# Kernel optimization log

Measured on AMD Instinct MI355X. Metric: run time of the kernel, lower is better.

The kernel has to match this reference:

```python
import jax, jax.numpy as jnp
import numpy as np

N_NODES = 100000
N_EDGES = 3200000
F_IN = 128
HID = 32
N_CLASSES = 40
NEG_SLOPE = 0.2


def _add_self_loops(edge_index, n):
    loops = jnp.arange(n, dtype=edge_index.dtype)
    src = jnp.concatenate([edge_index[0], loops])
    dst = jnp.concatenate([edge_index[1], loops])
    return src, dst


def _gat_layer(x, src, dst, W, a_src, a_dst, b, n):
    # h: [N, C]
    h = x @ W
    hs = h[src]                      # [E, C] gathered source features
    alpha_s = hs @ a_src             # [E]
    alpha_d = (h @ a_dst)[dst]       # [E]
    e = jax.nn.leaky_relu(alpha_s + alpha_d, NEG_SLOPE)
    # segment softmax over incoming edges per destination node
    m = jax.ops.segment_max(e, dst, num_segments=n)
    ex = jnp.exp(e - m[dst])
    denom = jax.ops.segment_sum(ex, dst, num_segments=n)
    alpha = ex / denom[dst]
    out = jax.ops.segment_sum(alpha[:, None] * hs, dst, num_segments=n)
    return out + b


def setup_inputs() -> dict:
    key = jax.random.key(0)
    ks = jax.random.split(key, 8)
    x = jax.random.normal(ks[0], (N_NODES, F_IN), dtype=jnp.float32)
    edge_index = jax.random.randint(ks[1], (2, N_EDGES), 0, N_NODES, dtype=jnp.int32)
    W1 = jax.random.normal(ks[2], (F_IN, HID), dtype=jnp.float32) * (1.0 / np.sqrt(F_IN))
    att_src1 = jax.random.normal(ks[3], (HID,), dtype=jnp.float32) * 0.1
    att_dst1 = jax.random.normal(ks[4], (HID,), dtype=jnp.float32) * 0.1
    b1 = jnp.zeros((HID,), dtype=jnp.float32)
    W2 = jax.random.normal(ks[5], (HID, N_CLASSES), dtype=jnp.float32) * (1.0 / np.sqrt(HID))
    att_src2 = jax.random.normal(ks[6], (N_CLASSES,), dtype=jnp.float32) * 0.1
    att_dst2 = jax.random.normal(ks[7], (N_CLASSES,), dtype=jnp.float32) * 0.1
    b2 = jnp.zeros((N_CLASSES,), dtype=jnp.float32)
    return {"x": x, "edge_index": edge_index, "W1": W1, "att_src1": att_src1,
            "att_dst1": att_dst1, "b1": b1, "W2": W2, "att_src2": att_src2,
            "att_dst2": att_dst2, "b2": b2}


def reference(x, edge_index, W1, att_src1, att_dst1, b1, W2, att_src2, att_dst2, b2):
    n = x.shape[0]
    src, dst = _add_self_loops(edge_index, n)  # PyG GATConv default add_self_loops=True
    h = _gat_layer(x, src, dst, W1, att_src1, att_dst1, b1, n)
    h = jax.nn.relu(h)  # dropout is identity in eval mode
    h = _gat_layer(h, src, dst, W2, att_src2, att_dst2, b2, n)
    h = jax.nn.relu(h)
    return jax.nn.log_softmax(h, axis=1)
```

## Files before the change

### kernel.cpp

```cpp
#include <hip/hip_runtime.h>
#include <hip/hip_bf16.h>
#include <hip/hip_fp16.h>
#include <math.h>

#define N_NODES 100000
#define N_EDGES 3200000
#define ET (N_EDGES + N_NODES)
#define F_IN 128
#define HID 32
#define NCLS 40
#define NEG 0.2f

#define NB 782
#define NBLK 782
#define CHUNK 4096
#define BCAP 6144
#define GEMM_BLKS (N_NODES / 8)

__global__ __launch_bounds__(256) void kA_hist(const int* __restrict__ dst,
                                               int* __restrict__ Hm) {
    __shared__ int hist[NB];
    int t = threadIdx.x, k = blockIdx.x;
    for (int i = t; i < NB; i += 256) hist[i] = 0;
    __syncthreads();
    int base = k * CHUNK;
#pragma unroll
    for (int j = 0; j < CHUNK / 256; j++) {
        int e = base + j * 256 + t;
        if (e < N_EDGES) atomicAdd(&hist[dst[e] >> 7], 1);
    }
    __syncthreads();
    for (int i = t; i < NB; i += 256) Hm[i * NBLK + k] = hist[i];
}

__global__ void k_scan_a(const int* __restrict__ in, int* __restrict__ out,
                         int* __restrict__ bsums, int L) {
    __shared__ int sd[256];
    int t = threadIdx.x, b = blockIdx.x;
    int base = b * 1024 + t * 4;
    int v0 = 0, v1 = 0, v2 = 0, v3 = 0;
    if (base     < L) v0 = in[base];
    if (base + 1 < L) v1 = in[base + 1];
    if (base + 2 < L) v2 = in[base + 2];
    if (base + 3 < L) v3 = in[base + 3];
    int ts = v0 + v1 + v2 + v3;
    sd[t] = ts;
    __syncthreads();
    for (int off = 1; off < 256; off <<= 1) {
        int xx = (t >= off) ? sd[t - off] : 0;
        __syncthreads();
        sd[t] += xx;
        __syncthreads();
    }
    int ex = sd[t] - ts;
    if (t == 255) bsums[b] = sd[255];
    if (base     < L) out[base]     = ex;
    if (base + 1 < L) out[base + 1] = ex + v0;
    if (base + 2 < L) out[base + 2] = ex + v0 + v1;
    if (base + 3 < L) out[base + 3] = ex + v0 + v1 + v2;
}

__global__ void k_scan_b(const int* __restrict__ bsums, int* __restrict__ boffs, int nb) {
    __shared__ int sd[256];
    int t = threadIdx.x;
    int base = t * 4;
    int v0 = 0, v1 = 0, v2 = 0, v3 = 0;
    if (base     < nb) v0 = bsums[base];
    if (base + 1 < nb) v1 = bsums[base + 1];
    if (base + 2 < nb) v2 = bsums[base + 2];
    if (base + 3 < nb) v3 = bsums[base + 3];
    int ts = v0 + v1 + v2 + v3;
    sd[t] = ts;
    __syncthreads();
    for (int off = 1; off < 256; off <<= 1) {
        int xx = (t >= off) ? sd[t - off] : 0;
        __syncthreads();
        sd[t] += xx;
        __syncthreads();
    }
    int ex = sd[t] - ts;
    if (base     < nb) boffs[base]     = ex;
    if (base + 1 < nb) boffs[base + 1] = ex + v0;
    if (base + 2 < nb) boffs[base + 2] = ex + v0 + v1;
    if (base + 3 < nb) boffs[base + 3] = ex + v0 + v1 + v2;
}

__global__ void k_scan_c(int* __restrict__ out, const int* __restrict__ boffs, int L) {
    int i = blockIdx.x * 256 + threadIdx.x;
    if (i < L) out[i] += boffs[i >> 10];
}

__global__ __launch_bounds__(256) void kA_scatter(
    const int* __restrict__ src, const int* __restrict__ dst,
    const int* __restrict__ Sx, unsigned int* __restrict__ tmp) {
    __shared__ int hist[NB];
    __shared__ int lofs[NB];
    __shared__ int tsum[256];
    __shared__ unsigned int stage[CHUNK];
    __shared__ unsigned short bkt16[CHUNK];
    int t = threadIdx.x, k = blockIdx.x;
    for (int i = t; i < NB; i += 256) hist[i] = 0;
    __syncthreads();
    int base = k * CHUNK;
    int myd[16], mys[16];
#pragma unroll
    for (int j = 0; j < 16; j++) {
        int e = base + j * 256 + t;
        myd[j] = (e < N_EDGES) ? dst[e] : -1;
        mys[j] = (e < N_EDGES) ? src[e] : 0;
        if (myd[j] >= 0) atomicAdd(&hist[myd[j] >> 7], 1);
    }
    __syncthreads();
    int i0 = 4 * t;
    int h0 = (i0     < NB) ? hist[i0]     : 0;
    int h1 = (i0 + 1 < NB) ? hist[i0 + 1] : 0;
    int h2 = (i0 + 2 < NB) ? hist[i0 + 2] : 0;
    int h3 = (i0 + 3 < NB) ? hist[i0 + 3] : 0;
    int ts = h0 + h1 + h2 + h3;
    tsum[t] = ts;
    __syncthreads();
    for (int off = 1; off < 256; off <<= 1) {
        int xx = (t >= off) ? tsum[t - off] : 0;
        __syncthreads();
        tsum[t] += xx;
        __syncthreads();
    }
    int ex = tsum[t] - ts;
    if (i0     < NB) { lofs[i0]     = ex;                hist[i0]     = 0; }
    if (i0 + 1 < NB) { lofs[i0 + 1] = ex + h0;           hist[i0 + 1] = 0; }
    if (i0 + 2 < NB) { lofs[i0 + 2] = ex + h0 + h1;      hist[i0 + 2] = 0; }
    if (i0 + 3 < NB) { lofs[i0 + 3] = ex + h0 + h1 + h2; hist[i0 + 3] = 0; }
    __syncthreads();
#pragma unroll
    for (int j = 0; j < 16; j++) {
        if (myd[j] >= 0) {
            int bkt = myd[j] >> 7;
            int slot = lofs[bkt] + atomicAdd(&hist[bkt], 1);
            stage[slot] = ((unsigned int)(myd[j] & 127) << 17) | (unsigned int)mys[j];
            bkt16[slot] = (unsigned short)bkt;
        }
    }
    __syncthreads();
    int nvalid = min(CHUNK, N_EDGES - base);
    for (int i = t; i < nvalid; i += 256) {
        int b = bkt16[i];
        tmp[Sx[b * NBLK + k] + (i - lofs[b])] = stage[i];
    }
}

__global__ __launch_bounds__(256) void kB_sort(
    const unsigned int* __restrict__ tmp, const int* __restrict__ Sx,
    int* __restrict__ esrc, int* __restrict__ rs, int* __restrict__ deg) {
    __shared__ unsigned int stage[BCAP];
    __shared__ int ordered[BCAP + 128];
    __shared__ int cnt[128], lofs[128], cur[128], sc[128];
    int t = threadIdx.x, b = blockIdx.x;
    int myBase = Sx[b * NBLK];
    int nextBase = (b == NB - 1) ? N_EDGES : Sx[(b + 1) * NBLK];
    int cntE = nextBase - myBase;
    int nNodes = min(128, N_NODES - b * 128);
    if (t < 128) { cnt[t] = 0; cur[t] = 0; }
    __syncthreads();
    for (int i = t; i < cntE; i += 256) {
        unsigned int p = tmp[myBase + i];
        stage[i] = p;
        atomicAdd(&cnt[p >> 17], 1);
    }
    __syncthreads();
    int val = 0;
    if (t < 128) { val = (t < nNodes) ? cnt[t] + 1 : 0; sc[t] = val; }
    __syncthreads();
    for (int off = 1; off < 128; off <<= 1) {
        int xx = 0;
        if (t < 128 && t >= off) xx = sc[t - off];
        __syncthreads();
        if (t < 128) sc[t] += xx;
        __syncthreads();
    }
    if (t < 128) lofs[t] = sc[t] - val;
    __syncthreads();
    if (t < nNodes) ordered[lofs[t]] = b * 128 + t;
    for (int i = t; i < cntE; i += 256) {
        unsigned int p = stage[i];
        int n = p >> 17;
        int slot = lofs[n] + 1 + atomicAdd(&cur[n], 1);
        ordered[slot] = (int)(p & 0x1FFFF);
    }
    __syncthreads();
    int gb = myBase + b * 128;
    int totOut = cntE + nNodes;
    for (int i = t; i < totOut; i += 256) esrc[gb + i] = ordered[i];
    if (t < nNodes) {
        rs[b * 128 + t] = gb + lofs[t];
        deg[b * 128 + t] = cnt[t] + 1;
    }
}

__global__ __launch_bounds__(256) void k_gemm1(
    const float* __restrict__ x, const float* __restrict__ W1,
    const float* __restrict__ a_s, const float* __restrict__ a_d,
    __half* __restrict__ h1h, float* __restrict__ s1, float* __restrict__ d1,
    const float* __restrict__ W2, const float* __restrict__ as2,
    const float* __restrict__ ad2, float* __restrict__ va_s, float* __restrict__ va_d) {
    __shared__ float Ws[F_IN * HID];
    __shared__ float xs[8 * F_IN];
    int t = threadIdx.x;
    if (blockIdx.x == GEMM_BLKS) {
        if (t < HID) {
            float ps = 0.f, pd = 0.f;
            for (int c = 0; c < NCLS; c++) {
                float w = W2[t * NCLS + c];
                ps = fmaf(w, as2[c], ps);
                pd = fmaf(w, ad2[c], pd);
            }
            va_s[t] = ps;
            va_d[t] = pd;
        }
        return;
    }
    const float4* W4 = (const float4*)W1;
    float4* Ws4 = (float4*)Ws;
#pragma unroll
    for (int i = 0; i < F_IN * HID / 4 / 256; i++)
        Ws4[t + i * 256] = W4[t + i * 256];
    ((float4*)xs)[t] = ((const float4*)(x + (size_t)blockIdx.x * 8 * F_IN))[t];
    __syncthreads();
    int c = t & 31, g = t >> 5;
    int v = blockIdx.x * 8 + g;
    const float4* xg4 = (const float4*)(xs + g * F_IN);
    float acc = 0.f;
#pragma unroll
    for (int k4 = 0; k4 < F_IN / 4; k4++) {
        float4 xv = xg4[k4];
        int k = k4 * 4;
        acc = fmaf(xv.x, Ws[(k + 0) * HID + c], acc);
        acc = fmaf(xv.y, Ws[(k + 1) * HID + c], acc);
        acc = fmaf(xv.z, Ws[(k + 2) * HID + c], acc);
        acc = fmaf(xv.w, Ws[(k + 3) * HID + c], acc);
    }
    h1h[(size_t)v * HID + c] = __float2half(acc);
    float p = acc * a_s[c];
    float q = acc * a_d[c];
    for (int mm = 16; mm >= 1; mm >>= 1) {
        p += __shfl_xor(p, mm, 32);
        q += __shfl_xor(q, mm, 32);
    }
    if (c == 0) { s1[v] = p; d1[v] = q; }
}

#define GATHER_BODY(SARR, TABLE)                                                  \
    float a0 = 0.f, a1 = 0.f, a2 = 0.f, a3 = 0.f,                                 \
          a4 = 0.f, a5 = 0.f, a6 = 0.f, a7 = 0.f;                                 \
    float den = 0.f;                                                              \
    int t = 0;                                                                    \
    int nmain = cnt & ~15;                                                        \
    int sa0 = 0, sa1 = 0, sa2 = 0, sa3 = 0;                                       \
    float sv0 = 0.f, sv1 = 0.f, sv2 = 0.f, sv3 = 0.f;                             \
    if (nmain > 0) {                                                              \
        int p0 = start + e;                                                       \
        sa0 = esrc[p0];      sa1 = esrc[p0 + 4];                                  \
        sa2 = esrc[p0 + 8];  sa3 = esrc[p0 + 12];                                 \
        sv0 = SARR[sa0]; sv1 = SARR[sa1]; sv2 = SARR[sa2]; sv3 = SARR[sa3];       \
    }                                                                             \
    for (; t < nmain; t += 16) {                                                  \
        uint4 hv0 = TABLE[(size_t)sa0 * 4 + q];                                   \
        uint4 hv1 = TABLE[(size_t)sa1 * 4 + q];                                   \
        uint4 hv2 = TABLE[(size_t)sa2 * 4 + q];                                   \
        uint4 hv3 = TABLE[(size_t)sa3 * 4 + q];                                   \
        float e0 = sv0 + dval; e0 = (e0 >= 0.f) ? e0 : NEG * e0;                  \
        float e1 = sv1 + dval; e1 = (e1 >= 0.f) ? e1 : NEG * e1;                  \
        float e2 = sv2 + dval; e2 = (e2 >= 0.f) ? e2 : NEG * e2;                  \
        float e3 = sv3 + dval; e3 = (e3 >= 0.f) ? e3 : NEG * e3;                  \
        float w0 = __expf(e0);                                                    \
        float w1 = __expf(e1);                                                    \
        float w2 = __expf(e2);                                                    \
        float w3 = __expf(e3);                                                    \
        den += (w0 + w1) + (w2 + w3);                                             \
        int nt = t + 16;                                                          \
        if (nt < nmain) {                                                         \
            int p = start + nt + e;                                               \
            sa0 = esrc[p];      sa1 = esrc[p + 4];                                \
            sa2 = esrc[p + 8];  sa3 = esrc[p + 12];                               \
            sv0 = SARR[sa0]; sv1 = SARR[sa1]; sv2 = SARR[sa2]; sv3 = SARR[sa3];   \
        }                                                                         \
        ACC8(w0, hv0); ACC8(w1, hv1); ACC8(w2, hv2); ACC8(w3, hv3);               \
    }                                                                             \
    for (; t < cnt; t += 4) {                                                     \
        int idx = t + e;                                                          \
        int sa = 0;                                                               \
        float w = 0.f;                                                            \
        if (idx < cnt) {                                                          \
            sa = esrc[start + idx];                                               \
            float ev = SARR[sa] + dval;                                           \
            ev = (ev >= 0.f) ? ev : NEG * ev;                                     \
            w = __expf(ev);                                                       \
        }                                                                         \
        uint4 hv = TABLE[(size_t)sa * 4 + q];                                     \
        ACC8(w, hv);                                                              \
        den += w;                                                                 \
    }

#define ACC8(W, HV)                                                               \
    {                                                                             \
        float2 f0 = __half22float2(*(const __half2*)&(HV).x);                     \
        float2 f1 = __half22float2(*(const __half2*)&(HV).y);                     \
        float2 f2 = __half22float2(*(const __half2*)&(HV).z);                     \
        float2 f3 = __half22float2(*(const __half2*)&(HV).w);                     \
        a0 = fmaf((W), f0.x, a0); a1 = fmaf((W), f0.y, a1);                       \
        a2 = fmaf((W), f1.x, a2); a3 = fmaf((W), f1.y, a3);                       \
        a4 = fmaf((W), f2.x, a4); a5 = fmaf((W), f2.y, a5);                       \
        a6 = fmaf((W), f3.x, a6); a7 = fmaf((W), f3.y, a7);                       \
    }

__global__ __launch_bounds__(256) void k_fused1(
    const int* __restrict__ rs, const int* __restrict__ deg, const int* __restrict__ esrc,
    const uint4* __restrict__ h1r, const float* __restrict__ s1, const float* __restrict__ d1,
    const float* __restrict__ b1, const float* __restrict__ va_s, const float* __restrict__ va_d,
    uint4* __restrict__ hrr, float* __restrict__ s2, float* __restrict__ d2) {
    int tid = threadIdx.x;
    int sub = tid & 15;
    int q = sub & 3;
    int e = sub >> 2;
    int v = blockIdx.x * 16 + (tid >> 4);
    int start = rs[v];
    int cnt = deg[v];
    float dval = d1[v];
    GATHER_BODY(s1, h1r)
#pragma unroll
    for (int off = 4; off <= 8; off <<= 1) {
        a0 += __shfl_xor(a0, off); a1 += __shfl_xor(a1, off);
        a2 += __shfl_xor(a2, off); a3 += __shfl_xor(a3, off);
        a4 += __shfl_xor(a4, off); a5 += __shfl_xor(a5, off);
        a6 += __shfl_xor(a6, off); a7 += __shfl_xor(a7, off);
        den += __shfl_xor(den, off);
    }
    if (e == 0) {
        float iden = 1.f / den;
        const float4* b4 = (const float4*)(b1 + q * 8);
        float4 bA = b4[0], bB = b4[1];
        float o0 = fmaxf(a0 * iden + bA.x, 0.f);
        float o1 = fmaxf(a1 * iden + bA.y, 0.f);
        float o2 = fmaxf(a2 * iden + bA.z, 0.f);
        float o3 = fmaxf(a3 * iden + bA.w, 0.f);
        float o4 = fmaxf(a4 * iden + bB.x, 0.f);
        float o5 = fmaxf(a5 * iden + bB.y, 0.f);
        float o6 = fmaxf(a6 * iden + bB.z, 0.f);
        float o7 = fmaxf(a7 * iden + bB.w, 0.f);
        __half2 p0 = __floats2half2_rn(o0, o1);
        __half2 p1 = __floats2half2_rn(o2, o3);
        __half2 p2 = __floats2half2_rn(o4, o5);
        __half2 p3 = __floats2half2_rn(o6, o7);
        uint4 ov;
        ov.x = *(const unsigned int*)&p0;
        ov.y = *(const unsigned int*)&p1;
        ov.z = *(const unsigned int*)&p2;
        ov.w = *(const unsigned int*)&p3;
        hrr[(size_t)v * 4 + q] = ov;
        const float4* vs4 = (const float4*)(va_s + q * 8);
        const float4* vd4 = (const float4*)(va_d + q * 8);
        float4 sA = vs4[0], sB = vs4[1], dA = vd4[0], dB = vd4[1];
        float ps = o0 * sA.x + o1 * sA.y + o2 * sA.z + o3 * sA.w
                 + o4 * sB.x + o5 * sB.y + o6 * sB.z + o7 * sB.w;
        float pd = o0 * dA.x + o1 * dA.y + o2 * dA.z + o3 * dA.w
                 + o4 * dB.x + o5 * dB.y + o6 * dB.z + o7 * dB.w;
        ps += __shfl_xor(ps, 1); pd += __shfl_xor(pd, 1);
        ps += __shfl_xor(ps, 2); pd += __shfl_xor(pd, 2);
        if (q == 0) { s2[v] = ps; d2[v] = pd; }
    }
}

__global__ __launch_bounds__(256) void k_fused2(
    const int* __restrict__ rs, const int* __restrict__ deg, const int* __restrict__ esrc,
    const uint4* __restrict__ hrr, const float* __restrict__ s2, const float* __restrict__ d2,
    const float* __restrict__ W2, const float* __restrict__ b2, float* __restrict__ out) {
    __shared__ float W2s[HID * NCLS];
    __shared__ float hragg[16][HID + 1];
    __shared__ float zbuf[16][NCLS];
    __shared__ float gm[16], gl[16];
    int tid = threadIdx.x;
    for (int i = tid; i < HID * NCLS; i += 256) W2s[i] = W2[i];
    int sub = tid & 15;
    int q = sub & 3;
    int e = sub >> 2;
    int node = tid >> 4;
    int v = blockIdx.x * 16 + node;
    int start = rs[v];
    int cnt = deg[v];
    float dval = d2[v];
    GATHER_BODY(s2, hrr)
#pragma unroll
    for (int off = 4; off <= 8; off <<= 1) {
        a0 += __shfl_xor(a0, off); a1 += __shfl_xor(a1, off);
        a2 += __shfl_xor(a2, off); a3 += __shfl_xor(a3, off);
        a4 += __shfl_xor(a4, off); a5 += __shfl_xor(a5, off);
        a6 += __shfl_xor(a6, off); a7 += __shfl_xor(a7, off);
        den += __shfl_xor(den, off);
    }
    if (e == 0) {
        float iden = 1.f / den;
        int cb = q * 8;
        hragg[node][cb + 0] = a0 * iden;
        hragg[node][cb + 1] = a1 * iden;
        hragg[node][cb + 2] = a2 * iden;
        hragg[node][cb + 3] = a3 * iden;
        hragg[node][cb + 4] = a4 * iden;
        hragg[node][cb + 5] = a5 * iden;
        hragg[node][cb + 6] = a6 * iden;
        hragg[node][cb + 7] = a7 * iden;
    }
    __syncthreads();
    for (int oi = tid; oi < 16 * NCLS; oi += 256) {
        int n = oi / NCLS, c = oi % NCLS;
        float z = 0.f;
#pragma unroll
        for (int k = 0; k < HID; k++)
            z = fmaf(hragg[n][k], W2s[k * NCLS + c], z);
        zbuf[n][c] = fmaxf(z + b2[c], 0.f);
    }
    __syncthreads();
    if (tid < 64) {
        int n = tid >> 2, j = tid & 3;
        float mx = 0.f;
        for (int c = j; c < NCLS; c += 4) mx = fmaxf(mx, zbuf[n][c]);
        mx = fmaxf(mx, __shfl_xor(mx, 1));
        mx = fmaxf(mx, __shfl_xor(mx, 2));
        float se = 0.f;
        for (int c = j; c < NCLS; c += 4) se += __expf(zbuf[n][c] - mx);
        se += __shfl_xor(se, 1);
        se += __shfl_xor(se, 2);
        if (j == 0) { gm[n] = mx; gl[n] = logf(se); }
    }
    __syncthreads();
    for (int oi = tid; oi < 16 * NCLS; oi += 256) {
        int n = oi / NCLS, c = oi % NCLS;
        out[(size_t)(blockIdx.x * 16 + n) * NCLS + c] = zbuf[n][c] - gm[n] - gl[n];
    }
}


extern "C" void kernel_launch(void* const* d_in, const int* in_sizes, int n_in,
                              void* d_out, int out_size, void* d_ws, size_t ws_size,
                              hipStream_t stream) {
    (void)in_sizes; (void)n_in; (void)out_size; (void)ws_size;
    const float* x   = (const float*)d_in[0];
    const int*   ei  = (const int*)d_in[1];
    const float* W1  = (const float*)d_in[2];
    const float* as1 = (const float*)d_in[3];
    const float* ad1 = (const float*)d_in[4];
    const float* b1  = (const float*)d_in[5];
    const float* W2  = (const float*)d_in[6];
    const float* as2 = (const float*)d_in[7];
    const float* ad2 = (const float*)d_in[8];
    const float* b2  = (const float*)d_in[9];
    float* out = (float*)d_out;
    const int* srcA = ei;
    const int* dstA = ei + N_EDGES;

    char* w = (char*)d_ws;
    size_t off = 0;
    auto alloc = [&](size_t bytes) {
        char* p = w + off;
        off = (off + bytes + 255) & ~(size_t)255;
        return p;
    };
    int* esrc     = (int*)alloc((size_t)ET * 4);
    int* rs       = (int*)alloc((size_t)N_NODES * 4);
    int* deg      = (int*)alloc((size_t)N_NODES * 4);
    char* region1 = alloc((size_t)N_NODES * HID * 4);
    float* s1     = (float*)alloc((size_t)N_NODES * 4);
    float* d1     = (float*)alloc((size_t)N_NODES * 4);
    char* region2 = alloc((size_t)N_EDGES * 4 + 1024);
    float* s2     = (float*)alloc((size_t)N_NODES * 4);
    float* d2     = (float*)alloc((size_t)N_NODES * 4);
    float* va_s   = (float*)alloc(HID * 4);
    float* va_d   = (float*)alloc(HID * 4);
    int* bsums    = (int*)alloc(1024 * 4);
    int* boffs    = (int*)alloc(1024 * 4);

    const int L = NB * NBLK;
    int* Hm = (int*)region1;
    int* Sx = Hm + ((L + 63) & ~63);
    __half* h1h = (__half*)region1;
    unsigned int* tmp = (unsigned int*)region2;
    __half* hrt = (__half*)region2;

    int nb1 = (L + 1023) / 1024;
    hipLaunchKernelGGL(kA_hist, dim3(NBLK), dim3(256), 0, stream, dstA, Hm);
    hipLaunchKernelGGL(k_scan_a, dim3(nb1), dim3(256), 0, stream, Hm, Sx, bsums, L);
    hipLaunchKernelGGL(k_scan_b, dim3(1), dim3(256), 0, stream, bsums, boffs, nb1);
    hipLaunchKernelGGL(k_scan_c, dim3((L + 255) / 256), dim3(256), 0, stream, Sx, boffs, L);
    hipLaunchKernelGGL(kA_scatter, dim3(NBLK), dim3(256), 0, stream, srcA, dstA, Sx, tmp);
    hipLaunchKernelGGL(kB_sort, dim3(NB), dim3(256), 0, stream, tmp, Sx, esrc, rs, deg);
    hipLaunchKernelGGL(k_gemm1, dim3(GEMM_BLKS + 1), dim3(256), 0, stream, x, W1, as1, ad1,
                       h1h, s1, d1, W2, as2, ad2, va_s, va_d);
    hipLaunchKernelGGL(k_fused1, dim3(N_NODES / 16), dim3(256), 0, stream, rs, deg, esrc,
                       (const uint4*)h1h, s1, d1, b1, va_s, va_d,
                       (uint4*)hrt, s2, d2);
    hipLaunchKernelGGL(k_fused2, dim3(N_NODES / 16), dim3(256), 0, stream, rs, deg, esrc,
                       (const uint4*)hrt, s2, d2, W2, b2, out);
}
```

Before: 319.0 us.

## Use nontemporal loads/stores, drop LDS staging in sort, remove gather prefetch

After: 339.5 us. 6.4% more time.

```diff
diff --git a/kernel.cpp b/kernel.cpp
--- a/kernel.cpp
+++ b/kernel.cpp
@@ -14,7 +14,7 @@
 #define NB 782
 #define NBLK 782
 #define CHUNK 4096
-#define BCAP 6144
+#define BCAP 5120
 #define GEMM_BLKS (N_NODES / 8)
 
 __global__ __launch_bounds__(256) void kA_hist(const int* __restrict__ dst,
@@ -27,7 +27,7 @@
 #pragma unroll
     for (int j = 0; j < CHUNK / 256; j++) {
         int e = base + j * 256 + t;
-        if (e < N_EDGES) atomicAdd(&hist[dst[e] >> 7], 1);
+        if (e < N_EDGES) atomicAdd(&hist[__builtin_nontemporal_load(&dst[e]) >> 7], 1);
     }
     __syncthreads();
     for (int i = t; i < NB; i += 256) Hm[i * NBLK + k] = hist[i];
@@ -106,8 +106,8 @@
 #pragma unroll
     for (int j = 0; j < 16; j++) {
         int e = base + j * 256 + t;
-        myd[j] = (e < N_EDGES) ? dst[e] : -1;
-        mys[j] = (e < N_EDGES) ? src[e] : 0;
+        myd[j] = (e < N_EDGES) ? __builtin_nontemporal_load(&dst[e]) : -1;
+        mys[j] = (e < N_EDGES) ? __builtin_nontemporal_load(&src[e]) : 0;
         if (myd[j] >= 0) atomicAdd(&hist[myd[j] >> 7], 1);
     }
     __syncthreads();
@@ -151,7 +151,6 @@
 __global__ __launch_bounds__(256) void kB_sort(
     const unsigned int* __restrict__ tmp, const int* __restrict__ Sx,
     int* __restrict__ esrc, int* __restrict__ rs, int* __restrict__ deg) {
-    __shared__ unsigned int stage[BCAP];
     __shared__ int ordered[BCAP + 128];
     __shared__ int cnt[128], lofs[128], cur[128], sc[128];
     int t = threadIdx.x, b = blockIdx.x;
@@ -163,7 +162,6 @@
     __syncthreads();
     for (int i = t; i < cntE; i += 256) {
         unsigned int p = tmp[myBase + i];
-        stage[i] = p;
         atomicAdd(&cnt[p >> 17], 1);
     }
     __syncthreads();
@@ -181,7 +179,7 @@
     __syncthreads();
     if (t < nNodes) ordered[lofs[t]] = b * 128 + t;
     for (int i = t; i < cntE; i += 256) {
-        unsigned int p = stage[i];
+        unsigned int p = tmp[myBase + i];
         int n = p >> 17;
         int slot = lofs[n] + 1 + atomicAdd(&cur[n], 1);
         ordered[slot] = (int)(p & 0x1FFFF);
@@ -253,16 +251,16 @@
           a4 = 0.f, a5 = 0.f, a6 = 0.f, a7 = 0.f;                                 \
     float den = 0.f;                                                              \
     int t = 0;                                                                    \
-    int nmain = cnt & ~15;                                                        \
-    int sa0 = 0, sa1 = 0, sa2 = 0, sa3 = 0;                                       \
-    float sv0 = 0.f, sv1 = 0.f, sv2 = 0.f, sv3 = 0.f;                             \
-    if (nmain > 0) {                                                              \
-        int p0 = start + e;                                                       \
-        sa0 = esrc[p0];      sa1 = esrc[p0 + 4];                                  \
-        sa2 = esrc[p0 + 8];  sa3 = esrc[p0 + 12];                                 \
-        sv0 = SARR[sa0]; sv1 = SARR[sa1]; sv2 = SARR[sa2]; sv3 = SARR[sa3];       \
-    }                                                                             \
-    for (; t < nmain; t += 16) {                                                  \
+    for (; t + 16 <= cnt; t += 16) {                                              \
+        int p0 = start + t + e;                                                   \
+        int sa0 = __builtin_nontemporal_load(&esrc[p0]);                          \
+        int sa1 = __builtin_nontemporal_load(&esrc[p0 + 4]);                      \
+        int sa2 = __builtin_nontemporal_load(&esrc[p0 + 8]);                      \
+        int sa3 = __builtin_nontemporal_load(&esrc[p0 + 12]);                     \
+        float sv0 = SARR[sa0];                                                    \
+        float sv1 = SARR[sa1];                                                    \
+        float sv2 = SARR[sa2];                                                    \
+        float sv3 = SARR[sa3];                                                    \
         uint4 hv0 = TABLE[(size_t)sa0 * 4 + q];                                   \
         uint4 hv1 = TABLE[(size_t)sa1 * 4 + q];                                   \
         uint4 hv2 = TABLE[(size_t)sa2 * 4 + q];                                   \
@@ -276,13 +274,6 @@
         float w2 = __expf(e2);                                                    \
         float w3 = __expf(e3);                                                    \
         den += (w0 + w1) + (w2 + w3);                                             \
-        int nt = t + 16;                                                          \
-        if (nt < nmain) {                                                         \
-            int p = start + nt + e;                                               \
-            sa0 = esrc[p];      sa1 = esrc[p + 4];                                \
-            sa2 = esrc[p + 8];  sa3 = esrc[p + 12];                               \
-            sv0 = SARR[sa0]; sv1 = SARR[sa1]; sv2 = SARR[sa2]; sv3 = SARR[sa3];   \
-        }                                                                         \
         ACC8(w0, hv0); ACC8(w1, hv1); ACC8(w2, hv2); ACC8(w3, hv3);               \
     }                                                                             \
     for (; t < cnt; t += 4) {                                                     \
@@ -290,7 +281,7 @@
         int sa = 0;                                                               \
         float w = 0.f;                                                            \
         if (idx < cnt) {                                                          \
-            sa = esrc[start + idx];                                               \
+            sa = __builtin_nontemporal_load(&esrc[start + idx]);                  \
             float ev = SARR[sa] + dval;                                           \
             ev = (ev >= 0.f) ? ev : NEG * ev;                                     \
             w = __expf(ev);                                                       \
@@ -433,7 +424,8 @@
     __syncthreads();
     for (int oi = tid; oi < 16 * NCLS; oi += 256) {
         int n = oi / NCLS, c = oi % NCLS;
-        out[(size_t)(blockIdx.x * 16 + n) * NCLS + c] = zbuf[n][c] - gm[n] - gl[n];
+        __builtin_nontemporal_store(zbuf[n][c] - gm[n] - gl[n],
+                                    &out[(size_t)(blockIdx.x * 16 + n) * NCLS + c]);
     }
 }
 
```
